# Kernel tuning notes

Hardware: AMD Instinct MI355X
Metric: run time of the kernel (lower is better)

Reference implementation:

```python
import jax, jax.numpy as jnp
import numpy as np

N_NODES = 100000
N_EDGES = 1600000
D = 64


def setup_inputs() -> dict:
    key = jax.random.key(0)
    k1, k2, k3 = jax.random.split(key, 3)
    x = jax.random.normal(k1, (N_NODES, D), dtype=jnp.float32)
    edge_index = jax.random.randint(k2, (2, N_EDGES), 0, N_NODES, dtype=jnp.int32)
    W = jax.random.normal(k3, (D, D), dtype=jnp.float32) * 0.05  # linear weight [out_dim, in_dim]
    b = jnp.zeros((D,), dtype=jnp.float32)
    return {"x": x, "edge_index": edge_index, "W": W, "b": b}


def reference(x, edge_index, W, b):
    n = x.shape[0]
    # add self loops
    loops = jnp.arange(n, dtype=edge_index.dtype)
    src = jnp.concatenate([edge_index[0], loops])
    dst = jnp.concatenate([edge_index[1], loops])
    # in-degree (counting self loops) via scatter-add of ones onto dst
    deg = jax.ops.segment_sum(jnp.ones_like(src, dtype=x.dtype), dst, num_segments=n)
    deg_inv_sqrt = jnp.where(deg > 0, jax.lax.rsqrt(jnp.maximum(deg, 1.0)) * (deg > 0), 0.0)
    deg_inv_sqrt = jnp.where(deg > 0, deg ** -0.5, 0.0)
    # per-edge symmetric normalization, gather-scale-scatter
    norm = deg_inv_sqrt[src] * deg_inv_sqrt[dst]  # [E+N]
    msgs = x[src] * norm[:, None]                  # [E+N, D] big irregular gather
    out = jax.ops.segment_sum(msgs, dst, num_segments=n)  # scatter-add to nodes
    # dense linear
    return out @ W.T + b
```

## Files before the change

### kernel.cpp

```cpp
#include <hip/hip_runtime.h>


#define BSHIFT 7
#define BNODES 128
#define CAP 3072
#define EPB 4096
#define SMEM_BYTES 32768

typedef short bf16x8 __attribute__((ext_vector_type(8)));
typedef float f32x4 __attribute__((ext_vector_type(4)));

__device__ inline unsigned short f2b_rn(float f) {
    unsigned u = __float_as_uint(f);
    unsigned r = u + 0x7FFFu + ((u >> 16) & 1u);
    return (unsigned short)(r >> 16);
}
__device__ inline float b2f(unsigned short h) {
    return __uint_as_float(((unsigned)h) << 16);
}

__device__ inline void split8(float4 a, float4 b, bf16x8* hi, bf16x8* lo) {
    float f[8] = {a.x, a.y, a.z, a.w, b.x, b.y, b.z, b.w};
    union U { unsigned u[4]; bf16x8 v; } uh, ul;
#pragma unroll
    for (int i = 0; i < 4; ++i) {
        unsigned u0 = __float_as_uint(f[2 * i]);
        unsigned u1 = __float_as_uint(f[2 * i + 1]);
        uh.u[i] = (u0 >> 16) | (u1 & 0xFFFF0000u);
        float r0 = f[2 * i]     - __uint_as_float(u0 & 0xFFFF0000u);
        float r1 = f[2 * i + 1] - __uint_as_float(u1 & 0xFFFF0000u);
        unsigned v0 = __float_as_uint(r0);
        unsigned v1 = __float_as_uint(r1);
        ul.u[i] = (v0 >> 16) | (v1 & 0xFFFF0000u);
    }
    *hi = uh.v;
    *lo = ul.v;
}

__global__ __launch_bounds__(256) void fused_gemm_scatter_kernel(
    const float* __restrict__ x, const float* __restrict__ W,
    ushort4* __restrict__ yh,
    const int* __restrict__ ei, int* __restrict__ gcur,
    unsigned int* __restrict__ grec,
    int n, int e, int nbuck, int sblocks) {
    __shared__ __align__(16) unsigned char smem[SMEM_BYTES];
    int t = threadIdx.x;

    if ((int)blockIdx.x < sblocks) {
        unsigned int* lrec = (unsigned int*)smem;
        unsigned short* lbk = (unsigned short*)(smem + 16384);
        int* lh = (int*)(smem + 24576);
        int* lbase = lh + nbuck;
        for (int i = t; i < nbuck; i += 256) lh[i] = 0;
        __syncthreads();
        int e0 = blockIdx.x * EPB;
        int m = e - e0;
        if (m > EPB) m = EPB;
        for (int i = t; i < m; i += 256) {
            int g = e0 + i;
            int s = ei[g];
            int d = ei[e + g];
            int b = d >> BSHIFT;
            lrec[i] = ((unsigned int)s << BSHIFT) | (unsigned int)(d & (BNODES - 1));
            lbk[i] = (unsigned short)b;
            atomicAdd(&lh[b], 1);
        }
        __syncthreads();
        for (int b = t; b < nbuck; b += 256) {
            int c = lh[b];
            lbase[b] = c ? atomicAdd(&gcur[b], c) : 0;
            lh[b] = 0;
        }
        __syncthreads();
        for (int i = t; i < m; i += 256) {
            int b = lbk[i];
            int pos = lbase[b] + atomicAdd(&lh[b], 1);
            if (pos < CAP)
                grec[(size_t)b * CAP + pos] = lrec[i];
        }
    } else {
        int wave = t >> 6, lane = t & 63;
        int jn = lane & 15;
        int g = lane >> 4;
        int node = ((int)blockIdx.x - sblocks) * 64 + wave * 16 + jn;

        bf16x8 xhi[2], xlo[2];
#pragma unroll
        for (int kb = 0; kb < 2; ++kb) {
            float4 p0 = {0.f, 0.f, 0.f, 0.f}, p1 = {0.f, 0.f, 0.f, 0.f};
            if (node < n) {
                const float4* xp =
                    (const float4*)(x + (size_t)node * 64 + kb * 32 + g * 8);
                p0 = xp[0];
                p1 = xp[1];
            }
            split8(p0, p1, &xhi[kb], &xlo[kb]);
        }

#pragma unroll
        for (int tt = 0; tt < 4; ++tt) {
            f32x4 acc = {0.f, 0.f, 0.f, 0.f};
#pragma unroll
            for (int kb = 0; kb < 2; ++kb) {
                const float4* wp =
                    (const float4*)(W + (size_t)(tt * 16 + jn) * 64 + kb * 32 + g * 8);
                float4 q0 = wp[0];
                float4 q1 = wp[1];
                bf16x8 whi, wlo;
                split8(q0, q1, &whi, &wlo);
                acc = __builtin_amdgcn_mfma_f32_16x16x32_bf16(wlo, xhi[kb], acc, 0, 0, 0);
                acc = __builtin_amdgcn_mfma_f32_16x16x32_bf16(whi, xlo[kb], acc, 0, 0, 0);
                acc = __builtin_amdgcn_mfma_f32_16x16x32_bf16(whi, xhi[kb], acc, 0, 0, 0);
            }
            if (node < n) {
                ushort4 h;
                h.x = f2b_rn(acc[0]);
                h.y = f2b_rn(acc[1]);
                h.z = f2b_rn(acc[2]);
                h.w = f2b_rn(acc[3]);
                yh[(size_t)node * 16 + (tt * 4 + g)] = h;
            }
        }
    }
}

__global__ __launch_bounds__(256) void dnorm_kernel(
    const unsigned int* __restrict__ grec, const int* __restrict__ gcur,
    float* __restrict__ dnorm, int n) {
    __shared__ int lh[BNODES];
    int t = threadIdx.x;
    int b = blockIdx.x;
    size_t base = (size_t)b * CAP;
    int cnt = gcur[b];
    if (cnt > CAP) cnt = CAP;
    if (t < BNODES) lh[t] = 0;
    __syncthreads();
    for (int i = t; i < cnt; i += 256)
        atomicAdd(&lh[grec[base + i] & (BNODES - 1)], 1);
    __syncthreads();
    if (t < BNODES) {
        int node = (b << BSHIFT) + t;
        if (node < n) dnorm[node] = rsqrtf((float)lh[t] + 1.0f);
    }
}

__global__ __launch_bounds__(512, 4) void csr_gather_kernel(
    const unsigned int* __restrict__ grec, const int* __restrict__ gcur,
    const ushort4* __restrict__ yh, const float* __restrict__ dnorm,
    const float* __restrict__ bias,
    float4* __restrict__ out, int n) {
    __shared__ unsigned int sorted[CAP];
    __shared__ int lh[BNODES];
    __shared__ int ls[BNODES + 1];
    __shared__ int wtot;
    int t = threadIdx.x;
    int b = blockIdx.x;
    size_t base = (size_t)b * CAP;
    int cnt = gcur[b];
    if (cnt > CAP) cnt = CAP;
    int node0 = b << BSHIFT;

    if (t < BNODES) lh[t] = 0;
    __syncthreads();
    for (int i = t; i < cnt; i += 512)
        atomicAdd(&lh[grec[base + i] & (BNODES - 1)], 1);
    __syncthreads();
    int c = 0, ex = 0;
    if (t < BNODES) {
        c = lh[t];
        int lane64 = t & 63;
        int v = c;
#pragma unroll
        for (int o = 1; o < 64; o <<= 1) {
            int u = __shfl_up(v, o, 64);
            if (lane64 >= o) v += u;
        }
        if (t == 63) wtot = v;
        ex = v - c;
    }
    __syncthreads();
    if (t >= 64 && t < BNODES) ex += wtot;
    if (t < BNODES) {
        ls[t] = ex;
        lh[t] = 0;
        if (t == BNODES - 1) ls[BNODES] = ex + c;
    }
    __syncthreads();
    for (int i = t; i < cnt; i += 512) {
        unsigned int r = grec[base + i];
        int nd = r & (BNODES - 1);
        int pos = ls[nd] + atomicAdd(&lh[nd], 1);
        sorted[pos] = r >> BSHIFT;
    }
    __syncthreads();

    int wave = t >> 6;
    int lane = t & 63;
    int grp = lane >> 4;
    int fq = lane & 15;
    float4 bb = ((const float4*)bias)[fq];
    for (int i = 0; i < 16; ++i) {
        int nd = wave * 16 + i;
        int node = node0 + nd;
        if (node >= n) break;
        int beg = ls[nd];
        int end = ls[nd + 1];
        float dn = rsqrtf((float)(end - beg) + 1.0f);
        float4 acc = {0.f, 0.f, 0.f, 0.f};
        if (grp == 0) {
            ushort4 h = yh[(size_t)node * 16 + fq];
            acc.x = dn * b2f(h.x); acc.y = dn * b2f(h.y);
            acc.z = dn * b2f(h.z); acc.w = dn * b2f(h.w);
        }
        int j = beg + grp;
        for (; j + 12 < end; j += 16) {
            int s0 = (int)sorted[j];
            int s1 = (int)sorted[j + 4];
            int s2 = (int)sorted[j + 8];
            int s3 = (int)sorted[j + 12];
            ushort4 h0 = yh[(size_t)s0 * 16 + fq];
            ushort4 h1 = yh[(size_t)s1 * 16 + fq];
            ushort4 h2 = yh[(size_t)s2 * 16 + fq];
            ushort4 h3 = yh[(size_t)s3 * 16 + fq];
            float d0 = dnorm[s0];
            float d1 = dnorm[s1];
            float d2 = dnorm[s2];
            float d3 = dnorm[s3];
            acc.x += d0 * b2f(h0.x); acc.x += d1 * b2f(h1.x);
            acc.x += d2 * b2f(h2.x); acc.x += d3 * b2f(h3.x);
            acc.y += d0 * b2f(h0.y); acc.y += d1 * b2f(h1.y);
            acc.y += d2 * b2f(h2.y); acc.y += d3 * b2f(h3.y);
            acc.z += d0 * b2f(h0.z); acc.z += d1 * b2f(h1.z);
            acc.z += d2 * b2f(h2.z); acc.z += d3 * b2f(h3.z);
            acc.w += d0 * b2f(h0.w); acc.w += d1 * b2f(h1.w);
            acc.w += d2 * b2f(h2.w); acc.w += d3 * b2f(h3.w);
        }
        for (; j < end; j += 4) {
            int s = (int)sorted[j];
            ushort4 h = yh[(size_t)s * 16 + fq];
            float d0 = dnorm[s];
            acc.x += d0 * b2f(h.x); acc.y += d0 * b2f(h.y);
            acc.z += d0 * b2f(h.z); acc.w += d0 * b2f(h.w);
        }
        for (int m = 16; m < 64; m <<= 1) {
            acc.x += __shfl_xor(acc.x, m);
            acc.y += __shfl_xor(acc.y, m);
            acc.z += __shfl_xor(acc.z, m);
            acc.w += __shfl_xor(acc.w, m);
        }
        if (lane < 16) {
            float4 o;
            o.x = acc.x * dn + bb.x;
            o.y = acc.y * dn + bb.y;
            o.z = acc.z * dn + bb.z;
            o.w = acc.w * dn + bb.w;
            out[(size_t)node * 16 + lane] = o;
        }
    }
}

extern "C" void kernel_launch(void* const* d_in, const int* in_sizes, int n_in,
                              void* d_out, int out_size, void* d_ws, size_t ws_size,
                              hipStream_t stream) {
    const float* x    = (const float*)d_in[0];
    const int*   ei   = (const int*)d_in[1];
    const float* W    = (const float*)d_in[2];
    const float* bias = (const float*)d_in[3];
    float* out = (float*)d_out;

    int n = in_sizes[0] / 64;
    int e = in_sizes[1] / 2;
    int nbuck = (n + BNODES - 1) / BNODES;

    auto align = [](size_t v) { return (v + 255) & ~(size_t)255; };
    char* p = (char*)d_ws;
    int* gcur = (int*)p;                    p += align((size_t)nbuck * 4);
    unsigned int* grec = (unsigned int*)p;  p += align((size_t)nbuck * CAP * 4);
    float* dnorm = (float*)p;               p += align((size_t)n * 4);
    ushort4* yh = (ushort4*)p;

    int sblocks = (e + EPB - 1) / EPB;
    int gblocks = (n + 63) / 64;

    hipMemsetAsync(gcur, 0, (size_t)nbuck * 4, stream);
    fused_gemm_scatter_kernel<<<sblocks + gblocks, 256, 0, stream>>>(
        x, W, yh, ei, gcur, grec, n, e, nbuck, sblocks);
    dnorm_kernel<<<nbuck, 256, 0, stream>>>(grec, gcur, dnorm, n);
    csr_gather_kernel<<<nbuck, 512, 0, stream>>>(grec, gcur, yh, dnorm, bias,
                                                 (float4*)out, n);
}
```

Baseline: 163.2 us.

## Fold source degree normalization into GEMM output and drop dnorm gathers

Splits the fused scatter/GEMM kernel into a scatter kernel followed by a GEMM kernel. The GEMM kernel computes each node's degree from its bucket and pre-scales its transformed row by that node's inverse square-root degree before storing it as bf16. The gather kernel then sums pre-scaled rows directly, removing the per-edge random dnorm loads and the separate dnorm kernel. In exchange the GEMM can no longer overlap with the scatter, because it must wait for scatter to finish, and it also reads the edge buckets again. W is now split once per block into shared memory.

```diff
diff --git a/kernel.cpp b/kernel.cpp
--- a/kernel.cpp
+++ b/kernel.cpp
@@ -5,7 +5,6 @@
 #define BNODES 128
 #define CAP 3072
 #define EPB 4096
-#define SMEM_BYTES 32768
 
 typedef short bf16x8 __attribute__((ext_vector_type(8)));
 typedef float f32x4 __attribute__((ext_vector_type(4)));
@@ -37,117 +36,120 @@
     *lo = ul.v;
 }
 
-__global__ __launch_bounds__(256) void fused_gemm_scatter_kernel(
+__global__ __launch_bounds__(256) void scatter_kernel(
+    const int* __restrict__ ei, int* __restrict__ gcur,
+    unsigned int* __restrict__ grec, int e, int nbuck) {
+    __shared__ unsigned int lrec[EPB];
+    __shared__ unsigned short lbk[EPB];
+    __shared__ int lh[1024];
+    __shared__ int lbase[1024];
+    int t = threadIdx.x;
+    for (int i = t; i < nbuck; i += 256) lh[i] = 0;
+    __syncthreads();
+    int e0 = blockIdx.x * EPB;
+    int m = e - e0;
+    if (m > EPB) m = EPB;
+    for (int i = t; i < m; i += 256) {
+        int g = e0 + i;
+        int s = ei[g];
+        int d = ei[e + g];
+        int b = d >> BSHIFT;
+        lrec[i] = ((unsigned int)s << BSHIFT) | (unsigned int)(d & (BNODES - 1));
+        lbk[i] = (unsigned short)b;
+        atomicAdd(&lh[b], 1);
+    }
+    __syncthreads();
+    for (int b = t; b < nbuck; b += 256) {
+        int c = lh[b];
+        lbase[b] = c ? atomicAdd(&gcur[b], c) : 0;
+        lh[b] = 0;
+    }
+    __syncthreads();
+    for (int i = t; i < m; i += 256) {
+        int b = lbk[i];
+        int pos = lbase[b] + atomicAdd(&lh[b], 1);
+        if (pos < CAP)
+            grec[(size_t)b * CAP + pos] = lrec[i];
+    }
+}
+
+__global__ __launch_bounds__(512) void gemm_scaled_kernel(
     const float* __restrict__ x, const float* __restrict__ W,
     ushort4* __restrict__ yh,
-    const int* __restrict__ ei, int* __restrict__ gcur,
-    unsigned int* __restrict__ grec,
-    int n, int e, int nbuck, int sblocks) {
-    __shared__ __align__(16) unsigned char smem[SMEM_BYTES];
-    int t = threadIdx.x;
-
-    if ((int)blockIdx.x < sblocks) {
-        unsigned int* lrec = (unsigned int*)smem;
-        unsigned short* lbk = (unsigned short*)(smem + 16384);
-        int* lh = (int*)(smem + 24576);
-        int* lbase = lh + nbuck;
-        for (int i = t; i < nbuck; i += 256) lh[i] = 0;
-        __syncthreads();
-        int e0 = blockIdx.x * EPB;
-        int m = e - e0;
-        if (m > EPB) m = EPB;
-        for (int i = t; i < m; i += 256) {
-            int g = e0 + i;
-            int s = ei[g];
-            int d = ei[e + g];
-            int b = d >> BSHIFT;
-            lrec[i] = ((unsigned int)s << BSHIFT) | (unsigned int)(d & (BNODES - 1));
-            lbk[i] = (unsigned short)b;
-            atomicAdd(&lh[b], 1);
-        }
-        __syncthreads();
-        for (int b = t; b < nbuck; b += 256) {
-            int c = lh[b];
-            lbase[b] = c ? atomicAdd(&gcur[b], c) : 0;
-            lh[b] = 0;
-        }
-        __syncthreads();
-        for (int i = t; i < m; i += 256) {
-            int b = lbk[i];
-            int pos = lbase[b] + atomicAdd(&lh[b], 1);
-            if (pos < CAP)
-                grec[(size_t)b * CAP + pos] = lrec[i];
-        }
-    } else {
-        int wave = t >> 6, lane = t & 63;
-        int jn = lane & 15;
-        int g = lane >> 4;
-        int node = ((int)blockIdx.x - sblocks) * 64 + wave * 16 + jn;
-
-        bf16x8 xhi[2], xlo[2];
-#pragma unroll
-        for (int kb = 0; kb < 2; ++kb) {
-            float4 p0 = {0.f, 0.f, 0.f, 0.f}, p1 = {0.f, 0.f, 0.f, 0.f};
-            if (node < n) {
-                const float4* xp =
-                    (const float4*)(x + (size_t)node * 64 + kb * 32 + g * 8);
-                p0 = xp[0];
-                p1 = xp[1];
-            }
-            split8(p0, p1, &xhi[kb], &xlo[kb]);
-        }
-
-#pragma unroll
-        for (int tt = 0; tt < 4; ++tt) {
-            f32x4 acc = {0.f, 0.f, 0.f, 0.f};
-#pragma unroll
-            for (int kb = 0; kb < 2; ++kb) {
-                const float4* wp =
-                    (const float4*)(W + (size_t)(tt * 16 + jn) * 64 + kb * 32 + g * 8);
-                float4 q0 = wp[0];
-                float4 q1 = wp[1];
-                bf16x8 whi, wlo;
-                split8(q0, q1, &whi, &wlo);
-                acc = __builtin_amdgcn_mfma_f32_16x16x32_bf16(wlo, xhi[kb], acc, 0, 0, 0);
-                acc = __builtin_amdgcn_mfma_f32_16x16x32_bf16(whi, xlo[kb], acc, 0, 0, 0);
-                acc = __builtin_amdgcn_mfma_f32_16x16x32_bf16(whi, xhi[kb], acc, 0, 0, 0);
-            }
-            if (node < n) {
-                ushort4 h;
-                h.x = f2b_rn(acc[0]);
-                h.y = f2b_rn(acc[1]);
-                h.z = f2b_rn(acc[2]);
-                h.w = f2b_rn(acc[3]);
-                yh[(size_t)node * 16 + (tt * 4 + g)] = h;
-            }
-        }
-    }
-}
-
-__global__ __launch_bounds__(256) void dnorm_kernel(
     const unsigned int* __restrict__ grec, const int* __restrict__ gcur,
-    float* __restrict__ dnorm, int n) {
+    int n) {
+    __shared__ bf16x8 Whi[512];
+    __shared__ bf16x8 Wlo[512];
     __shared__ int lh[BNODES];
     int t = threadIdx.x;
     int b = blockIdx.x;
+    int node0 = b << BSHIFT;
+
+    if (t < BNODES) lh[t] = 0;
+    __syncthreads();
+
     size_t base = (size_t)b * CAP;
     int cnt = gcur[b];
     if (cnt > CAP) cnt = CAP;
-    if (t < BNODES) lh[t] = 0;
-    __syncthreads();
-    for (int i = t; i < cnt; i += 256)
+    for (int i = t; i < cnt; i += 512)
         atomicAdd(&lh[grec[base + i] & (BNODES - 1)], 1);
-    __syncthreads();
-    if (t < BNODES) {
-        int node = (b << BSHIFT) + t;
-        if (node < n) dnorm[node] = rsqrtf((float)lh[t] + 1.0f);
+
+    {
+        int tt = t >> 7, kb = (t >> 6) & 1, g = (t >> 4) & 3, jn = t & 15;
+        const float4* wp =
+            (const float4*)(W + (size_t)(tt * 16 + jn) * 64 + kb * 32 + g * 8);
+        bf16x8 hi, lo;
+        split8(wp[0], wp[1], &hi, &lo);
+        Whi[t] = hi;
+        Wlo[t] = lo;
+    }
+    __syncthreads();
+
+    int wave = t >> 6, lane = t & 63;
+    int jn = lane & 15;
+    int g = lane >> 4;
+    int node = node0 + wave * 16 + jn;
+
+    bf16x8 xhi[2], xlo[2];
+#pragma unroll
+    for (int kb = 0; kb < 2; ++kb) {
+        float4 p0 = {0.f, 0.f, 0.f, 0.f}, p1 = {0.f, 0.f, 0.f, 0.f};
+        if (node < n) {
+            const float4* xp =
+                (const float4*)(x + (size_t)node * 64 + kb * 32 + g * 8);
+            p0 = xp[0];
+            p1 = xp[1];
+        }
+        split8(p0, p1, &xhi[kb], &xlo[kb]);
+    }
+
+    float dn = rsqrtf((float)lh[wave * 16 + jn] + 1.0f);
+
+#pragma unroll
+    for (int tt = 0; tt < 4; ++tt) {
+        f32x4 acc = {0.f, 0.f, 0.f, 0.f};
+#pragma unroll
+        for (int kb = 0; kb < 2; ++kb) {
+            bf16x8 whi = Whi[(tt * 2 + kb) * 64 + lane];
+            bf16x8 wlo = Wlo[(tt * 2 + kb) * 64 + lane];
+            acc = __builtin_amdgcn_mfma_f32_16x16x32_bf16(wlo, xhi[kb], acc, 0, 0, 0);
+            acc = __builtin_amdgcn_mfma_f32_16x16x32_bf16(whi, xlo[kb], acc, 0, 0, 0);
+            acc = __builtin_amdgcn_mfma_f32_16x16x32_bf16(whi, xhi[kb], acc, 0, 0, 0);
+        }
+        if (node < n) {
+            ushort4 h;
+            h.x = f2b_rn(acc[0] * dn);
+            h.y = f2b_rn(acc[1] * dn);
+            h.z = f2b_rn(acc[2] * dn);
+            h.w = f2b_rn(acc[3] * dn);
+            yh[(size_t)node * 16 + (tt * 4 + g)] = h;
+        }
     }
 }
 
 __global__ __launch_bounds__(512, 4) void csr_gather_kernel(
     const unsigned int* __restrict__ grec, const int* __restrict__ gcur,
-    const ushort4* __restrict__ yh, const float* __restrict__ dnorm,
-    const float* __restrict__ bias,
+    const ushort4* __restrict__ yh, const float* __restrict__ bias,
     float4* __restrict__ out, int n) {
     __shared__ unsigned int sorted[CAP];
     __shared__ int lh[BNODES];
@@ -209,8 +211,8 @@
         float4 acc = {0.f, 0.f, 0.f, 0.f};
         if (grp == 0) {
             ushort4 h = yh[(size_t)node * 16 + fq];
-            acc.x = dn * b2f(h.x); acc.y = dn * b2f(h.y);
-            acc.z = dn * b2f(h.z); acc.w = dn * b2f(h.w);
+            acc.x = b2f(h.x); acc.y = b2f(h.y);
+            acc.z = b2f(h.z); acc.w = b2f(h.w);
         }
         int j = beg + grp;
         for (; j + 12 < end; j += 16) {
@@ -222,25 +224,16 @@
             ushort4 h1 = yh[(size_t)s1 * 16 + fq];
             ushort4 h2 = yh[(size_t)s2 * 16 + fq];
             ushort4 h3 = yh[(size_t)s3 * 16 + fq];
-            float d0 = dnorm[s0];
-            float d1 = dnorm[s1];
-            float d2 = dnorm[s2];
-            float d3 = dnorm[s3];
-            acc.x += d0 * b2f(h0.x); acc.x += d1 * b2f(h1.x);
-            acc.x += d2 * b2f(h2.x); acc.x += d3 * b2f(h3.x);
-            acc.y += d0 * b2f(h0.y); acc.y += d1 * b2f(h1.y);
-            acc.y += d2 * b2f(h2.y); acc.y += d3 * b2f(h3.y);
-            acc.z += d0 * b2f(h0.z); acc.z += d1 * b2f(h1.z);
-            acc.z += d2 * b2f(h2.z); acc.z += d3 * b2f(h3.z);
-            acc.w += d0 * b2f(h0.w); acc.w += d1 * b2f(h1.w);
-            acc.w += d2 * b2f(h2.w); acc.w += d3 * b2f(h3.w);
+            acc.x += b2f(h0.x) + b2f(h1.x) + b2f(h2.x) + b2f(h3.x);
+            acc.y += b2f(h0.y) + b2f(h1.y) + b2f(h2.y) + b2f(h3.y);
+            acc.z += b2f(h0.z) + b2f(h1.z) + b2f(h2.z) + b2f(h3.z);
+            acc.w += b2f(h0.w) + b2f(h1.w) + b2f(h2.w) + b2f(h3.w);
         }
         for (; j < end; j += 4) {
             int s = (int)sorted[j];
             ushort4 h = yh[(size_t)s * 16 + fq];
-            float d0 = dnorm[s];
-            acc.x += d0 * b2f(h.x); acc.y += d0 * b2f(h.y);
-            acc.z += d0 * b2f(h.z); acc.w += d0 * b2f(h.w);
+            acc.x += b2f(h.x); acc.y += b2f(h.y);
+            acc.z += b2f(h.z); acc.w += b2f(h.w);
         }
         for (int m = 16; m < 64; m <<= 1) {
             acc.x += __shfl_xor(acc.x, m);
@@ -276,16 +269,13 @@
     char* p = (char*)d_ws;
     int* gcur = (int*)p;                    p += align((size_t)nbuck * 4);
     unsigned int* grec = (unsigned int*)p;  p += align((size_t)nbuck * CAP * 4);
-    float* dnorm = (float*)p;               p += align((size_t)n * 4);
     ushort4* yh = (ushort4*)p;
 
     int sblocks = (e + EPB - 1) / EPB;
-    int gblocks = (n + 63) / 64;
 
     hipMemsetAsync(gcur, 0, (size_t)nbuck * 4, stream);
-    fused_gemm_scatter_kernel<<<sblocks + gblocks, 256, 0, stream>>>(
-        x, W, yh, ei, gcur, grec, n, e, nbuck, sblocks);
-    dnorm_kernel<<<nbuck, 256, 0, stream>>>(grec, gcur, dnorm, n);
-    csr_gather_kernel<<<nbuck, 512, 0, stream>>>(grec, gcur, yh, dnorm, bias,
+    scatter_kernel<<<sblocks, 256, 0, stream>>>(ei, gcur, grec, e, nbuck);
+    gemm_scaled_kernel<<<nbuck, 512, 0, stream>>>(x, W, yh, grec, gcur, n);
+    csr_gather_kernel<<<nbuck, 512, 0, stream>>>(grec, gcur, yh, bias,
                                                  (float4*)out, n);
 }
```

Result: no change. 160.3 us (-1.8%).
